# Performance work log

Measured on AMD Instinct MI355X. Metric: run time of the kernel, lower is better.

The kernel has to match this reference:

```python
import jax, jax.numpy as jnp
from jax import lax
import numpy as np


def _relu(x):
    return jnp.maximum(x, 0)


def setup_inputs() -> dict:
    key = jax.random.key(0)
    ks = jax.random.split(key, 20)
    B = 1024
    s = 0.05  # small init scale
    d = {
        "raw_input": jax.random.normal(ks[0], (B, 1, 28, 28), jnp.float32),
        "output_embed": jax.random.normal(ks[1], (B, 512), jnp.float32),
        "latent_embed": jax.random.normal(ks[2], (B, 512), jnp.float32),
        "conv1_w": jax.random.normal(ks[3], (16, 1, 3, 3), jnp.float32) * s,
        "conv1_b": jax.random.normal(ks[4], (16,), jnp.float32) * s,
        "conv2_w": jax.random.normal(ks[5], (32, 16, 3, 3), jnp.float32) * s,
        "conv2_b": jax.random.normal(ks[6], (32,), jnp.float32) * s,
        "proj_w1": jax.random.normal(ks[7], (1568, 1024), jnp.float32) * s,
        "proj_b1": jax.random.normal(ks[8], (1024,), jnp.float32) * s,
        "proj_w2": jax.random.normal(ks[9], (1024, 512), jnp.float32) * s,
        "proj_b2": jax.random.normal(ks[10], (512,), jnp.float32) * s,
        "bb_w1": jax.random.normal(ks[11], (512, 1024), jnp.float32) * s,
        "bb_b1": jax.random.normal(ks[12], (1024,), jnp.float32) * s,
        "bb_w2": jax.random.normal(ks[13], (1024, 512), jnp.float32) * s,
        "bb_b2": jax.random.normal(ks[14], (512,), jnp.float32) * s,
        "head_w": jax.random.normal(ks[15], (512, 10), jnp.float32) * s,
        "head_b": jax.random.normal(ks[16], (10,), jnp.float32) * s,
        "Nsup": 16,
        "n_latent": 6,
    }
    return d


def _maxpool2(x):
    # 2x2 max pool, stride 2, NCHW
    return lax.reduce_window(x, -jnp.inf, lax.max, (1, 1, 2, 2), (1, 1, 2, 2), "VALID")


def reference(raw_input, output_embed, latent_embed,
              conv1_w, conv1_b, conv2_w, conv2_b,
              proj_w1, proj_b1, proj_w2, proj_b2,
              bb_w1, bb_b1, bb_w2, bb_b2,
              head_w, head_b, Nsup, n_latent):
    dn = ("NCHW", "OIHW", "NCHW")
    B = raw_input.shape[0]

    def backbone(x):
        return _relu(_relu(x @ bb_w1 + bb_b1) @ bb_w2 + bb_b2)

    def latent_recursion(inp, out, lat, n):
        if n > 0:
            for _ in range(n):
                lat = backbone(inp + out + lat)
            out = backbone(lat + inp)
        else:
            out = backbone(inp + out + lat)
        return out, lat

    # CNN extractor + input embedding projection (B, 512)
    x = _relu(lax.conv_general_dilated(raw_input, conv1_w, (1, 1), "SAME",
                                       dimension_numbers=dn) + conv1_b[None, :, None, None])
    x = _maxpool2(x)  # (B,16,14,14)
    x = _relu(lax.conv_general_dilated(x, conv2_w, (1, 1), "SAME",
                                       dimension_numbers=dn) + conv2_b[None, :, None, None])
    x = _maxpool2(x)  # (B,32,7,7)
    h = x.reshape(B, -1)  # (B, 1568)
    inp = _relu(_relu(h @ proj_w1 + proj_b1) @ proj_w2 + proj_b2)  # (B,512)

    sg = lax.stop_gradient
    out, lat = output_embed, latent_embed
    T = 3
    logits = None
    for _ in range(Nsup):
        # deep_recursion: T-1 no-grad latent recursions, then one tracked
        for _ in range(T - 1):
            out, lat = latent_recursion(inp, out, lat, n_latent)
            out, lat = sg(out), sg(lat)
        out, lat = latent_recursion(inp, out, lat, n_latent)
        logits = out @ head_w + head_b
        out, lat = sg(out), sg(lat)
    return logits
```

## Files before the change

### kernel.cpp

```cpp
#include <hip/hip_runtime.h>
#include <hip/hip_bf16.h>


typedef unsigned short ushort_t;
typedef __attribute__((ext_vector_type(8))) short short8;
typedef __attribute__((ext_vector_type(4))) float f32x4;

__device__ inline unsigned f2bf_rne(float v) {
    unsigned u = __float_as_uint(v);
    return (u + 0x7fffu + ((u >> 16) & 1u)) >> 16;
}
__device__ inline void split2(float v, ushort_t& h, ushort_t& l) {
    unsigned uh = f2bf_rne(v);
    h = (ushort_t)uh;
    float fh = __uint_as_float(uh << 16);
    l = (ushort_t)f2bf_rne(v - fh);
}

__global__ __launch_bounds__(256) void conv1_pool(
    const float* __restrict__ in, const float* __restrict__ w,
    const float* __restrict__ bias, float* __restrict__ out)
{
    int idx = blockIdx.x * 256 + threadIdx.x;
    int xo = idx % 14; int t = idx / 14;
    int yo = t % 14;  t /= 14;
    int oc = t % 16;  int b = t / 16;
    const float* ip = in + (size_t)b * 784;
    const float* wp = w + oc * 9;
    float win[4][4];
#pragma unroll
    for (int yy = 0; yy < 4; ++yy)
#pragma unroll
        for (int xx = 0; xx < 4; ++xx) {
            int y = 2 * yo + yy - 1, x = 2 * xo + xx - 1;
            win[yy][xx] = (y >= 0 && y < 28 && x >= 0 && x < 28) ? ip[y * 28 + x] : 0.f;
        }
    float bs = bias[oc];
    float m = -1e30f;
#pragma unroll
    for (int py = 0; py < 2; ++py)
#pragma unroll
        for (int px = 0; px < 2; ++px) {
            float s = bs;
#pragma unroll
            for (int dy = 0; dy < 3; ++dy)
#pragma unroll
                for (int dx = 0; dx < 3; ++dx)
                    s = fmaf(win[py + dy][px + dx], wp[dy * 3 + dx], s);
            m = fmaxf(m, s);
        }
    out[idx] = fmaxf(m, 0.f);
}

__global__ __launch_bounds__(256) void conv2_pool(
    const float* __restrict__ in, const float* __restrict__ w,
    const float* __restrict__ bias, float* __restrict__ out)
{
    __shared__ float ws_[32 * 16 * 9];
    for (int i = threadIdx.x; i < 4608; i += 256) ws_[i] = w[i];
    __syncthreads();
    int idx = blockIdx.x * 256 + threadIdx.x;
    int xo = idx % 7; int t = idx / 7;
    int yo = t % 7;  t /= 7;
    int oc = t % 32; int b = t / 32;
    const float* ip = in + (size_t)b * 16 * 196;
    float bs = bias[oc];
    float s00 = bs, s01 = bs, s10 = bs, s11 = bs;
    for (int ic = 0; ic < 16; ++ic) {
        const float* ipp = ip + ic * 196;
        float win[4][4];
#pragma unroll
        for (int yy = 0; yy < 4; ++yy)
#pragma unroll
            for (int xx = 0; xx < 4; ++xx) {
                int y = 2 * yo + yy - 1, x = 2 * xo + xx - 1;
                win[yy][xx] = (y >= 0 && y < 14 && x >= 0 && x < 14) ? ipp[y * 14 + x] : 0.f;
            }
        const float* wp = ws_ + (oc * 16 + ic) * 9;
#pragma unroll
        for (int dy = 0; dy < 3; ++dy)
#pragma unroll
            for (int dx = 0; dx < 3; ++dx) {
                float wv = wp[dy * 3 + dx];
                s00 = fmaf(win[0 + dy][0 + dx], wv, s00);
                s01 = fmaf(win[0 + dy][1 + dx], wv, s01);
                s10 = fmaf(win[1 + dy][0 + dx], wv, s10);
                s11 = fmaf(win[1 + dy][1 + dx], wv, s11);
            }
    }
    float m = fmaxf(fmaxf(s00, s01), fmaxf(s10, s11));
    out[idx] = fmaxf(m, 0.f);
}

#define BMF 64
#define BNF 64
#define BKF 16

__global__ __launch_bounds__(256) void gemm_f32(
    const float* __restrict__ A0, const float* __restrict__ W,
    const float* __restrict__ bias, float* __restrict__ C,
    int M, int N, int K)
{
    __shared__ float As[BKF][BMF];
    __shared__ float Bs[BKF][BNF];
    const int tid = threadIdx.x;
    const int tx = tid % 16;
    const int ty = tid / 16;
    const int row0 = blockIdx.y * BMF;
    const int col0 = blockIdx.x * BNF;
    float acc[4][4] = {};
    const int ra = tid / 4;
    const int ca = 4 * (tid % 4);
    const int rb = tid / 16;
    const int cb = 4 * (tid % 16);
    for (int k0 = 0; k0 < K; k0 += BKF) {
        float4 v = *(const float4*)(A0 + (size_t)(row0 + ra) * K + k0 + ca);
        float4 bvec = *(const float4*)(W + (size_t)(k0 + rb) * N + col0 + cb);
        As[ca + 0][ra] = v.x;
        As[ca + 1][ra] = v.y;
        As[ca + 2][ra] = v.z;
        As[ca + 3][ra] = v.w;
        *(float4*)&Bs[rb][cb] = bvec;
        __syncthreads();
#pragma unroll
        for (int kk = 0; kk < BKF; ++kk) {
            float4 av = *(const float4*)&As[kk][ty * 4];
            float4 bv = *(const float4*)&Bs[kk][tx * 4];
            float a_[4] = {av.x, av.y, av.z, av.w};
            float b_[4] = {bv.x, bv.y, bv.z, bv.w};
#pragma unroll
            for (int i = 0; i < 4; ++i)
#pragma unroll
                for (int j = 0; j < 4; ++j)
                    acc[i][j] = fmaf(a_[i], b_[j], acc[i][j]);
        }
        __syncthreads();
    }
    float4 bv = *(const float4*)(bias + col0 + tx * 4);
    float bb[4] = {bv.x, bv.y, bv.z, bv.w};
#pragma unroll
    for (int i = 0; i < 4; ++i) {
        float4 o;
        o.x = fmaxf(acc[i][0] + bb[0], 0.f);
        o.y = fmaxf(acc[i][1] + bb[1], 0.f);
        o.z = fmaxf(acc[i][2] + bb[2], 0.f);
        o.w = fmaxf(acc[i][3] + bb[3], 0.f);
        *(float4*)(C + (size_t)(row0 + ty * 4 + i) * N + col0 + tx * 4) = o;
    }
}

__global__ __launch_bounds__(256) void prep_wt(
    const float* __restrict__ w, ushort_t* __restrict__ th,
    ushort_t* __restrict__ tl, int K, int N)
{
    int idx = blockIdx.x * 256 + threadIdx.x;
    int n = idx / K, k = idx % K;
    float v = w[(size_t)k * N + n];
    split2(v, th[idx], tl[idx]);
}

__global__ __launch_bounds__(256) void init_xs(
    const float* __restrict__ inpf, const float* __restrict__ oute,
    const float* __restrict__ late, float* __restrict__ io,
    ushort_t* __restrict__ xh, ushort_t* __restrict__ xl)
{
    int i = blockIdx.x * 256 + threadIdx.x;
    float t = inpf[i] + oute[i];
    io[i] = t;
    split2(t + late[i], xh[i], xl[i]);
}

__global__ void init_bar(unsigned* bar) {
    bar[threadIdx.x] = 0;
    bar[threadIdx.x + 256] = 0;
}

__device__ __forceinline__ void group_barrier(unsigned* bar, int g,
                                              unsigned& tgt)
{
    __syncthreads();
    if (threadIdx.x == 0) {
        __builtin_amdgcn_fence(__ATOMIC_RELEASE, "workgroup");
        __hip_atomic_fetch_add(bar + g * 32, 1u, __ATOMIC_RELAXED,
                               __HIP_MEMORY_SCOPE_AGENT);
        while (__hip_atomic_load(bar + g * 32, __ATOMIC_RELAXED,
                                 __HIP_MEMORY_SCOPE_AGENT) < tgt)
            __builtin_amdgcn_s_sleep(1);
        __builtin_amdgcn_fence(__ATOMIC_ACQUIRE, "workgroup");
        asm volatile("buffer_inv sc0" ::: "memory");
    }
    tgt += 32;
    __syncthreads();
}

__device__ __forceinline__ short8 afrag(const ushort_t* __restrict__ p,
                                        int row, int K, int kpos)
{
    return *(const short8*)(p + (size_t)row * K + kpos);
}

__global__ __launch_bounds__(512, 2) void trm_persist(
    ushort_t* __restrict__ xs_hi, ushort_t* __restrict__ xs_lo,
    ushort_t* __restrict__ h1_hi, ushort_t* __restrict__ h1_lo,
    const ushort_t* __restrict__ W1h, const ushort_t* __restrict__ W1l,
    const ushort_t* __restrict__ W2h, const ushort_t* __restrict__ W2l,
    const float* __restrict__ bb1, const float* __restrict__ bb2,
    float* __restrict__ io, const float* __restrict__ inpf,
    float* __restrict__ latf, float* __restrict__ outf,
    const float* __restrict__ hw, const float* __restrict__ hb,
    float* __restrict__ logits, unsigned* bar)
{
    __shared__ __align__(16) unsigned char w1lds[65536];
    __shared__ __align__(16) unsigned char w2lds[65536];
    __shared__ int sh_gs;

    const int tid = threadIdx.x;
    const int w = tid >> 6, lane = tid & 63;
    const int q = lane >> 4, li = lane & 15;

    if (tid == 0) {
        unsigned xcc;
        asm volatile("s_getreg_b32 %0, hwreg(HW_REG_XCC_ID)" : "=s"(xcc));
        xcc &= 7u;
        unsigned s = __hip_atomic_fetch_add(bar + 384 + xcc * 8, 1u,
                                            __ATOMIC_RELAXED,
                                            __HIP_MEMORY_SCOPE_AGENT);
        sh_gs = (int)((xcc << 8) | (s & 31u));
    }
    __syncthreads();
    const int g = sh_gs >> 8;
    const int slot = sh_gs & 255;
    const int c1 = slot * 32;
    const int c2 = slot * 16;
    const int rowA = g * 128 + w * 16;

    for (int i = tid; i < 4096; i += 512) {
        int comp = i >> 11;
        int rem = i & 2047;
        int n = rem >> 6, c = rem & 63;
        const ushort_t* src = (comp ? W1l : W1h) + (size_t)(c1 + n) * 512 + c * 8;
        int dst = ((((comp << 4) + (c >> 2)) * 2 + (n >> 4)) * 64 +
                   ((c & 3) * 16 + (n & 15))) * 16;
        *(uint4*)(w1lds + dst) = *(const uint4*)src;
    }
    for (int i = tid; i < 4096; i += 512) {
        int comp = i >> 11;
        int rem = i & 2047;
        int n = rem >> 7, c = rem & 127;
        const ushort_t* src = (comp ? W2l : W2h) + (size_t)(c2 + n) * 1024 + c * 8;
        int dst = (((comp << 5) + (c >> 2)) * 64 + ((c & 3) * 16 + n)) * 16;
        *(uint4*)(w2lds + dst) = *(const uint4*)src;
    }
    __syncthreads();

    float bias1[2];
    bias1[0] = bb1[c1 + li];
    bias1[1] = bb1[c1 + 16 + li];
    float bias2 = bb2[c2 + li];
    unsigned tgt = 32;

    for (int step = 0; step < 336; ++step) {
        {
            f32x4 acc0 = {}, acc1 = {};
            short8 aF[8][2];
#pragma unroll
            for (int p = 0; p < 8; ++p) {
                int kp = p * 32 + q * 8;
                aF[p][0] = afrag(xs_hi, rowA + li, 512, kp);
                aF[p][1] = afrag(xs_lo, rowA + li, 512, kp);
            }
            __builtin_amdgcn_sched_barrier(0);
#pragma unroll
            for (int s = 0; s < 16; ++s) {
                short8 ah = aF[s & 7][0], al = aF[s & 7][1];
                if (s + 8 < 16) {
                    int kp = (s + 8) * 32 + q * 8;
                    aF[(s + 8) & 7][0] = afrag(xs_hi, rowA + li, 512, kp);
                    aF[(s + 8) & 7][1] = afrag(xs_lo, rowA + li, 512, kp);
                }
                __builtin_amdgcn_sched_barrier(0);
                const int base = (s * 2 * 64 + lane) * 16;
                short8 bh0 = *(const short8*)(w1lds + base);
                short8 bh1 = *(const short8*)(w1lds + base + 1024);
                short8 bl0 = *(const short8*)(w1lds + 32768 + base);
                short8 bl1 = *(const short8*)(w1lds + 32768 + base + 1024);
                acc0 = __builtin_amdgcn_mfma_f32_16x16x32_bf16(ah, bh0, acc0, 0, 0, 0);
                acc0 = __builtin_amdgcn_mfma_f32_16x16x32_bf16(ah, bl0, acc0, 0, 0, 0);
                acc0 = __builtin_amdgcn_mfma_f32_16x16x32_bf16(al, bh0, acc0, 0, 0, 0);
                acc0 = __builtin_amdgcn_mfma_f32_16x16x32_bf16(al, bl0, acc0, 0, 0, 0);
                acc1 = __builtin_amdgcn_mfma_f32_16x16x32_bf16(ah, bh1, acc1, 0, 0, 0);
                acc1 = __builtin_amdgcn_mfma_f32_16x16x32_bf16(ah, bl1, acc1, 0, 0, 0);
                acc1 = __builtin_amdgcn_mfma_f32_16x16x32_bf16(al, bh1, acc1, 0, 0, 0);
                acc1 = __builtin_amdgcn_mfma_f32_16x16x32_bf16(al, bl1, acc1, 0, 0, 0);
            }
#pragma unroll
            for (int tj = 0; tj < 2; ++tj) {
                int colg = c1 + tj * 16 + li;
                float bv = bias1[tj];
#pragma unroll
                for (int rr = 0; rr < 4; ++rr) {
                    int rowg = rowA + q * 4 + rr;
                    size_t idx = (size_t)rowg * 1024 + colg;
                    float v = fmaxf((tj ? acc1[rr] : acc0[rr]) + bv, 0.f);
                    split2(v, h1_hi[idx], h1_lo[idx]);
                }
            }
        }
        group_barrier(bar, g, tgt);

        {
            int im = step % 7;
            int mode = (im < 5) ? 1 : ((im == 5) ? 2 : 3);
            f32x4 acc = {};
            short8 aF[16][2];
#pragma unroll
            for (int p = 0; p < 16; ++p) {
                int kp = p * 32 + q * 8;
                aF[p][0] = afrag(h1_hi, rowA + li, 1024, kp);
                aF[p][1] = afrag(h1_lo, rowA + li, 1024, kp);
            }
            __builtin_amdgcn_sched_barrier(0);
#pragma unroll
            for (int s = 0; s < 32; ++s) {
                short8 ah = aF[s & 15][0], al = aF[s & 15][1];
                if (s + 16 < 32) {
                    int kp = (s + 16) * 32 + q * 8;
                    aF[(s + 16) & 15][0] = afrag(h1_hi, rowA + li, 1024, kp);
                    aF[(s + 16) & 15][1] = afrag(h1_lo, rowA + li, 1024, kp);
                }
                __builtin_amdgcn_sched_barrier(0);
                const int base = (s * 64 + lane) * 16;
                short8 bh = *(const short8*)(w2lds + base);
                short8 bl = *(const short8*)(w2lds + 32768 + base);
                acc = __builtin_amdgcn_mfma_f32_16x16x32_bf16(ah, bh, acc, 0, 0, 0);
                acc = __builtin_amdgcn_mfma_f32_16x16x32_bf16(ah, bl, acc, 0, 0, 0);
                acc = __builtin_amdgcn_mfma_f32_16x16x32_bf16(al, bh, acc, 0, 0, 0);
                acc = __builtin_amdgcn_mfma_f32_16x16x32_bf16(al, bl, acc, 0, 0, 0);
            }
            int colg = c2 + li;
#pragma unroll
            for (int rr = 0; rr < 4; ++rr) {
                int rowg = rowA + q * 4 + rr;
                size_t idx = (size_t)rowg * 512 + colg;
                float v = fmaxf(acc[rr] + bias2, 0.f);
                if (mode == 1) {
                    split2(io[idx] + v, xs_hi[idx], xs_lo[idx]);
                } else if (mode == 2) {
                    split2(inpf[idx] + v, xs_hi[idx], xs_lo[idx]);
                    latf[idx] = v;
                } else {
                    outf[idx] = v;
                    float t2 = inpf[idx] + v;
                    io[idx] = t2;
                    split2(t2 + latf[idx], xs_hi[idx], xs_lo[idx]);
                }
            }
        }
        group_barrier(bar, g, tgt);
    }

    {
        int idx = slot * 512 + tid;
        if (idx < 1280) {
            int rloc = idx / 10, j = idx % 10;
            int row = g * 128 + rloc;
            const float* r = outf + (size_t)row * 512;
            float s = hb[j];
            for (int k = 0; k < 512; ++k) s = fmaf(r[k], hw[k * 10 + j], s);
            logits[row * 10 + j] = s;
        }
    }
}

extern "C" void kernel_launch(void* const* d_in, const int* in_sizes, int n_in,
                              void* d_out, int out_size, void* d_ws, size_t ws_size,
                              hipStream_t stream)
{
    const float* raw   = (const float*)d_in[0];
    const float* out_e = (const float*)d_in[1];
    const float* lat_e = (const float*)d_in[2];
    const float* c1w = (const float*)d_in[3];
    const float* c1b = (const float*)d_in[4];
    const float* c2w = (const float*)d_in[5];
    const float* c2b = (const float*)d_in[6];
    const float* pw1 = (const float*)d_in[7];
    const float* pb1 = (const float*)d_in[8];
    const float* pw2 = (const float*)d_in[9];
    const float* pb2 = (const float*)d_in[10];
    const float* bw1 = (const float*)d_in[11];
    const float* bb1 = (const float*)d_in[12];
    const float* bw2 = (const float*)d_in[13];
    const float* bb2 = (const float*)d_in[14];
    const float* hw  = (const float*)d_in[15];
    const float* hb  = (const float*)d_in[16];

    char* base = (char*)d_ws;
    float*    pool1  = (float*)   (base + 0);
    ushort_t* h1_hi  = (ushort_t*)(base + 0);
    ushort_t* h1_lo  = (ushort_t*)(base + 2097152);
    ushort_t* xs_hi  = (ushort_t*)(base + 4194304);
    ushort_t* xs_lo  = (ushort_t*)(base + 5242880);
    float*    io     = (float*)   (base + 6291456);
    float*    latf   = (float*)   (base + 8388608);
    float*    h1f    = (float*)   (base + 0);
    float*    h      = (float*)   (base + 12845056);
    float*    inpf   = (float*)   (base + 19267584);
    float*    outf   = (float*)   (base + 21364736);
    ushort_t* bW1t_h = (ushort_t*)(base + 23461888);
    ushort_t* bW1t_l = (ushort_t*)(base + 24510464);
    ushort_t* bW2t_h = (ushort_t*)(base + 25559040);
    ushort_t* bW2t_l = (ushort_t*)(base + 26607616);
    unsigned* bar    = (unsigned*)(base + 27656192);

    prep_wt<<<2048, 256, 0, stream>>>(bw1, bW1t_h, bW1t_l, 512, 1024);
    prep_wt<<<2048, 256, 0, stream>>>(bw2, bW2t_h, bW2t_l, 1024, 512);

    conv1_pool<<<3211264 / 256, 256, 0, stream>>>(raw, c1w, c1b, pool1);
    conv2_pool<<<1605632 / 256, 256, 0, stream>>>(pool1, c2w, c2b, h);
    gemm_f32<<<dim3(16, 16), 256, 0, stream>>>(h, pw1, pb1, h1f, 1024, 1024, 1568);
    gemm_f32<<<dim3(8, 16), 256, 0, stream>>>(h1f, pw2, pb2, inpf, 1024, 512, 1024);
    init_xs<<<2048, 256, 0, stream>>>(inpf, out_e, lat_e, io, xs_hi, xs_lo);

    init_bar<<<1, 256, 0, stream>>>(bar);

    trm_persist<<<256, 512, 0, stream>>>(
        xs_hi, xs_lo, h1_hi, h1_lo, bW1t_h, bW1t_l, bW2t_h, bW2t_l,
        bb1, bb2, io, inpf, latf, outf, hw, hb, (float*)d_out, bar);
}
```

Before: 8.396 ms.

## Double workgroup waves and split GEMM work across two wave halves

```diff
diff --git a/kernel.cpp b/kernel.cpp
--- a/kernel.cpp
+++ b/kernel.cpp
@@ -199,7 +199,7 @@
     return *(const short8*)(p + (size_t)row * K + kpos);
 }
 
-__global__ __launch_bounds__(512, 2) void trm_persist(
+__global__ __launch_bounds__(1024, 4) void trm_persist(
     ushort_t* __restrict__ xs_hi, ushort_t* __restrict__ xs_lo,
     ushort_t* __restrict__ h1_hi, ushort_t* __restrict__ h1_lo,
     const ushort_t* __restrict__ W1h, const ushort_t* __restrict__ W1l,
@@ -212,11 +212,14 @@
 {
     __shared__ __align__(16) unsigned char w1lds[65536];
     __shared__ __align__(16) unsigned char w2lds[65536];
+    __shared__ __align__(16) f32x4 scr[512];
     __shared__ int sh_gs;
 
     const int tid = threadIdx.x;
     const int w = tid >> 6, lane = tid & 63;
     const int q = lane >> 4, li = lane & 15;
+    const int rw = w & 7;
+    const int hi_half = w >> 3;
 
     if (tid == 0) {
         unsigned xcc;
@@ -232,9 +235,9 @@
     const int slot = sh_gs & 255;
     const int c1 = slot * 32;
     const int c2 = slot * 16;
-    const int rowA = g * 128 + w * 16;
-
-    for (int i = tid; i < 4096; i += 512) {
+    const int rowA = g * 128 + rw * 16;
+
+    for (int i = tid; i < 4096; i += 1024) {
         int comp = i >> 11;
         int rem = i & 2047;
         int n = rem >> 6, c = rem & 63;
@@ -243,7 +246,7 @@
                    ((c & 3) * 16 + (n & 15))) * 16;
         *(uint4*)(w1lds + dst) = *(const uint4*)src;
     }
-    for (int i = tid; i < 4096; i += 512) {
+    for (int i = tid; i < 4096; i += 1024) {
         int comp = i >> 11;
         int rem = i & 2047;
         int n = rem >> 7, c = rem & 127;
@@ -253,15 +256,13 @@
     }
     __syncthreads();
 
-    float bias1[2];
-    bias1[0] = bb1[c1 + li];
-    bias1[1] = bb1[c1 + 16 + li];
+    float bias1v = bb1[c1 + hi_half * 16 + li];
     float bias2 = bb2[c2 + li];
     unsigned tgt = 32;
 
     for (int step = 0; step < 336; ++step) {
         {
-            f32x4 acc0 = {}, acc1 = {};
+            f32x4 acc = {};
             short8 aF[8][2];
 #pragma unroll
             for (int p = 0; p < 8; ++p) {
@@ -270,6 +271,7 @@
                 aF[p][1] = afrag(xs_lo, rowA + li, 512, kp);
             }
             __builtin_amdgcn_sched_barrier(0);
+            const int tjoff = hi_half * 1024;
 #pragma unroll
             for (int s = 0; s < 16; ++s) {
                 short8 ah = aF[s & 7][0], al = aF[s & 7][1];
@@ -279,31 +281,21 @@
                     aF[(s + 8) & 7][1] = afrag(xs_lo, rowA + li, 512, kp);
                 }
                 __builtin_amdgcn_sched_barrier(0);
-                const int base = (s * 2 * 64 + lane) * 16;
-                short8 bh0 = *(const short8*)(w1lds + base);
-                short8 bh1 = *(const short8*)(w1lds + base + 1024);
-                short8 bl0 = *(const short8*)(w1lds + 32768 + base);
-                short8 bl1 = *(const short8*)(w1lds + 32768 + base + 1024);
-                acc0 = __builtin_amdgcn_mfma_f32_16x16x32_bf16(ah, bh0, acc0, 0, 0, 0);
-                acc0 = __builtin_amdgcn_mfma_f32_16x16x32_bf16(ah, bl0, acc0, 0, 0, 0);
-                acc0 = __builtin_amdgcn_mfma_f32_16x16x32_bf16(al, bh0, acc0, 0, 0, 0);
-                acc0 = __builtin_amdgcn_mfma_f32_16x16x32_bf16(al, bl0, acc0, 0, 0, 0);
-                acc1 = __builtin_amdgcn_mfma_f32_16x16x32_bf16(ah, bh1, acc1, 0, 0, 0);
-                acc1 = __builtin_amdgcn_mfma_f32_16x16x32_bf16(ah, bl1, acc1, 0, 0, 0);
-                acc1 = __builtin_amdgcn_mfma_f32_16x16x32_bf16(al, bh1, acc1, 0, 0, 0);
-                acc1 = __builtin_amdgcn_mfma_f32_16x16x32_bf16(al, bl1, acc1, 0, 0, 0);
-            }
-#pragma unroll
-            for (int tj = 0; tj < 2; ++tj) {
-                int colg = c1 + tj * 16 + li;
-                float bv = bias1[tj];
-#pragma unroll
-                for (int rr = 0; rr < 4; ++rr) {
-                    int rowg = rowA + q * 4 + rr;
-                    size_t idx = (size_t)rowg * 1024 + colg;
-                    float v = fmaxf((tj ? acc1[rr] : acc0[rr]) + bv, 0.f);
-                    split2(v, h1_hi[idx], h1_lo[idx]);
-                }
+                const int base = (s * 2 * 64 + lane) * 16 + tjoff;
+                short8 bh = *(const short8*)(w1lds + base);
+                short8 bl = *(const short8*)(w1lds + 32768 + base);
+                acc = __builtin_amdgcn_mfma_f32_16x16x32_bf16(ah, bh, acc, 0, 0, 0);
+                acc = __builtin_amdgcn_mfma_f32_16x16x32_bf16(ah, bl, acc, 0, 0, 0);
+                acc = __builtin_amdgcn_mfma_f32_16x16x32_bf16(al, bh, acc, 0, 0, 0);
+                acc = __builtin_amdgcn_mfma_f32_16x16x32_bf16(al, bl, acc, 0, 0, 0);
+            }
+            int colg = c1 + hi_half * 16 + li;
+#pragma unroll
+            for (int rr = 0; rr < 4; ++rr) {
+                int rowg = rowA + q * 4 + rr;
+                size_t idx = (size_t)rowg * 1024 + colg;
+                float v = fmaxf(acc[rr] + bias1v, 0.f);
+                split2(v, h1_hi[idx], h1_lo[idx]);
             }
         }
         group_barrier(bar, g, tgt);
@@ -312,24 +304,25 @@
             int im = step % 7;
             int mode = (im < 5) ? 1 : ((im == 5) ? 2 : 3);
             f32x4 acc = {};
-            short8 aF[16][2];
-#pragma unroll
-            for (int p = 0; p < 16; ++p) {
-                int kp = p * 32 + q * 8;
+            short8 aF[8][2];
+            const int sb = hi_half * 16;
+#pragma unroll
+            for (int p = 0; p < 8; ++p) {
+                int kp = (sb + p) * 32 + q * 8;
                 aF[p][0] = afrag(h1_hi, rowA + li, 1024, kp);
                 aF[p][1] = afrag(h1_lo, rowA + li, 1024, kp);
             }
             __builtin_amdgcn_sched_barrier(0);
 #pragma unroll
-            for (int s = 0; s < 32; ++s) {
-                short8 ah = aF[s & 15][0], al = aF[s & 15][1];
-                if (s + 16 < 32) {
-                    int kp = (s + 16) * 32 + q * 8;
-                    aF[(s + 16) & 15][0] = afrag(h1_hi, rowA + li, 1024, kp);
-                    aF[(s + 16) & 15][1] = afrag(h1_lo, rowA + li, 1024, kp);
+            for (int s = 0; s < 16; ++s) {
+                short8 ah = aF[s & 7][0], al = aF[s & 7][1];
+                if (s + 8 < 16) {
+                    int kp = (sb + s + 8) * 32 + q * 8;
+                    aF[(s + 8) & 7][0] = afrag(h1_hi, rowA + li, 1024, kp);
+                    aF[(s + 8) & 7][1] = afrag(h1_lo, rowA + li, 1024, kp);
                 }
                 __builtin_amdgcn_sched_barrier(0);
-                const int base = (s * 64 + lane) * 16;
+                const int base = ((sb + s) * 64 + lane) * 16;
                 short8 bh = *(const short8*)(w2lds + base);
                 short8 bl = *(const short8*)(w2lds + 32768 + base);
                 acc = __builtin_amdgcn_mfma_f32_16x16x32_bf16(ah, bh, acc, 0, 0, 0);
@@ -337,22 +330,27 @@
                 acc = __builtin_amdgcn_mfma_f32_16x16x32_bf16(al, bh, acc, 0, 0, 0);
                 acc = __builtin_amdgcn_mfma_f32_16x16x32_bf16(al, bl, acc, 0, 0, 0);
             }
-            int colg = c2 + li;
-#pragma unroll
-            for (int rr = 0; rr < 4; ++rr) {
-                int rowg = rowA + q * 4 + rr;
-                size_t idx = (size_t)rowg * 512 + colg;
-                float v = fmaxf(acc[rr] + bias2, 0.f);
-                if (mode == 1) {
-                    split2(io[idx] + v, xs_hi[idx], xs_lo[idx]);
-                } else if (mode == 2) {
-                    split2(inpf[idx] + v, xs_hi[idx], xs_lo[idx]);
-                    latf[idx] = v;
-                } else {
-                    outf[idx] = v;
-                    float t2 = inpf[idx] + v;
-                    io[idx] = t2;
-                    split2(t2 + latf[idx], xs_hi[idx], xs_lo[idx]);
+            if (hi_half) scr[rw * 64 + lane] = acc;
+            __syncthreads();
+            if (!hi_half) {
+                acc += scr[rw * 64 + lane];
+                int colg = c2 + li;
+#pragma unroll
+                for (int rr = 0; rr < 4; ++rr) {
+                    int rowg = rowA + q * 4 + rr;
+                    size_t idx = (size_t)rowg * 512 + colg;
+                    float v = fmaxf(acc[rr] + bias2, 0.f);
+                    if (mode == 1) {
+                        split2(io[idx] + v, xs_hi[idx], xs_lo[idx]);
+                    } else if (mode == 2) {
+                        split2(inpf[idx] + v, xs_hi[idx], xs_lo[idx]);
+                        latf[idx] = v;
+                    } else {
+                        outf[idx] = v;
+                        float t2 = inpf[idx] + v;
+                        io[idx] = t2;
+                        split2(t2 + latf[idx], xs_hi[idx], xs_lo[idx]);
+                    }
                 }
             }
         }
@@ -360,7 +358,7 @@
     }
 
     {
-        int idx = slot * 512 + tid;
+        int idx = slot * 1024 + tid;
         if (idx < 1280) {
             int rloc = idx / 10, j = idx % 10;
             int row = g * 128 + rloc;
@@ -423,7 +421,7 @@
 
     init_bar<<<1, 256, 0, stream>>>(bar);
 
-    trm_persist<<<256, 512, 0, stream>>>(
+    trm_persist<<<256, 1024, 0, stream>>>(
         xs_hi, xs_lo, h1_hi, h1_lo, bW1t_h, bW1t_l, bW2t_h, bW2t_l,
         bb1, bb2, io, inpf, latf, outf, hw, hb, (float*)d_out, bar);
 }
```

Result: slower. 14.64 ms (+74.4%).
